# Performance work log

Measured on AMD Instinct MI355X. Metric: run time of the kernel, lower is better.

## Reference

```python
import jax, jax.numpy as jnp
import numpy as np
import math

B, T, D = 2, 2048, 1024
NH = 16
HD = D // NH


def setup_inputs() -> dict:
    key = jax.random.key(0)
    k1, k2, k3 = jax.random.split(key, 3)
    scale = 0.02
    x = jax.random.normal(k1, (B, T, D), dtype=jnp.float32)
    Wqkv = jax.random.normal(k2, (D, 3 * D), dtype=jnp.float32) * scale
    bqkv = jnp.zeros((3 * D,), dtype=jnp.float32)
    Wproj = jax.random.normal(k3, (D, D), dtype=jnp.float32) * scale
    bproj = jnp.zeros((D,), dtype=jnp.float32)
    return {"x": x, "Wqkv": Wqkv, "bqkv": bqkv, "Wproj": Wproj, "bproj": bproj}


def reference(x, Wqkv, bqkv, Wproj, bproj):
    b, t, c = x.shape
    qkv = x @ Wqkv + bqkv                      # [B,T,3D]
    q, k, v = jnp.split(qkv, 3, axis=2)
    # [B,T,NH,HD] -> [B,NH,T,HD]
    q = q.reshape(b, t, NH, HD).transpose(0, 2, 1, 3)
    k = k.reshape(b, t, NH, HD).transpose(0, 2, 1, 3)
    v = v.reshape(b, t, NH, HD).transpose(0, 2, 1, 3)
    att = jnp.einsum('bhqd,bhkd->bhqk', q, k) / math.sqrt(HD)  # [B,NH,T,T]
    causal = jnp.tril(jnp.ones((t, t), dtype=bool))
    att = jnp.where(causal, att, -jnp.inf)
    att = jax.nn.softmax(att, axis=-1)
    y = jnp.einsum('bhqk,bhkd->bhqd', att, v)  # [B,NH,T,HD]
    y = y.transpose(0, 2, 1, 3).reshape(b, t, c)
    return y @ Wproj + bproj
```

## Files before the change

kernel.cpp:

```cpp
#include <hip/hip_runtime.h>
#include <hip/hip_bf16.h>

#define B_   2
#define T_   2048
#define D_   1024
#define NH_  16
#define HD_  64
#define MROWS (B_*T_)
#define HEADELEMS (B_*NH_*T_*HD_)

#define QSCALE 0.180336880f

typedef unsigned short u16;
typedef unsigned int   u32;

typedef float f32x4  __attribute__((ext_vector_type(4)));
typedef short bf16x8 __attribute__((ext_vector_type(8)));

#define GLP(g, l) __builtin_amdgcn_global_load_lds(                         \
    (const __attribute__((address_space(1))) void*)(g),                     \
    (__attribute__((address_space(3))) void*)(l), 16, 0, 0)

struct Fc { static constexpr bool value = false; };
struct Tc { static constexpr bool value = true;  };

__device__ __forceinline__ u16 f2bf(float f) {
    u32 x = __float_as_uint(f);
    u32 r = (x + 0x7fffu + ((x >> 16) & 1u)) >> 16;
    return (u16)r;
}
__device__ __forceinline__ u32 pkbf2(float a, float b) {
    __hip_bfloat162 h = __float22bfloat162_rn(make_float2(a, b));
    union { __hip_bfloat162 h2; u32 u; } cv; cv.h2 = h; return cv.u;
}

__device__ __forceinline__ void transpose_tile(const float* in, u16* out,
                                               int K, int N, int bx, int by,
                                               int t, float (*Ts)[65])
{
    const int n0 = bx * 64;
    const int k0 = by * 64;
    #pragma unroll
    for (int pass = 0; pass < 4; pass++) {
        const int r = pass * 16 + (t >> 4);
        const int c = (t & 15) * 4;
        float4 v = *(const float4*)(in + (size_t)(k0 + r) * N + n0 + c);
        Ts[r][c] = v.x; Ts[r][c+1] = v.y; Ts[r][c+2] = v.z; Ts[r][c+3] = v.w;
    }
    __syncthreads();
    #pragma unroll
    for (int pass = 0; pass < 2; pass++) {
        const int nn = pass * 32 + (t >> 3);
        const int kk = (t & 7) * 8;
        u16 o[8];
        #pragma unroll
        for (int j = 0; j < 8; j++) o[j] = f2bf(Ts[kk + j][nn]);
        *(uint4*)(out + (size_t)(n0 + nn) * K + k0 + kk) = *(const uint4*)o;
    }
}

__global__ __launch_bounds__(256)
void prep_kernel(const float* __restrict__ x, const float* __restrict__ Wqkv,
                 const float* __restrict__ Wproj, u16* __restrict__ xb,
                 u16* __restrict__ WqkvT, u16* __restrict__ WprojT)
{
    __shared__ float Ts[64][65];
    const int bid = blockIdx.x;
    const int t   = threadIdx.x;
    if (bid < 4096) {
        int i = bid * 256 + t;
        float4 v = ((const float4*)x)[i];
        ushort4 o;
        o.x = f2bf(v.x); o.y = f2bf(v.y); o.z = f2bf(v.z); o.w = f2bf(v.w);
        ((ushort4*)xb)[i] = o;
    } else if (bid < 4096 + 768) {
        int tb = bid - 4096;
        transpose_tile(Wqkv, WqkvT, D_, 3*D_, tb % 48, tb / 48, t, Ts);
    } else {
        int tb = bid - 4864;
        transpose_tile(Wproj, WprojT, D_, D_, tb % 16, tb / 16, t, Ts);
    }
}

__global__ __launch_bounds__(256)
void transpose_conv_kernel(const float* __restrict__ in, u16* __restrict__ out,
                           int K, int N)
{
    __shared__ float Ts[64][65];
    transpose_tile(in, out, K, N, blockIdx.x, blockIdx.y, threadIdx.x, Ts);
}

template <int MODE>
__global__ __launch_bounds__(256)
void gemm_mfma(const u16* __restrict__ A, const u16* __restrict__ BT,
               const float* __restrict__ bias, void* __restrict__ outv,
               int M, int N, int K)
{
    __shared__ u16 As[128][64];
    __shared__ u16 Bs[128][64];

    const int t    = threadIdx.x;
    const int wave = t >> 6;
    const int lane = t & 63;
    const int l16  = lane & 15;
    const int quad = lane >> 4;

    const int m0 = blockIdx.y * 128;
    const int n0 = blockIdx.x * 128;
    const int mb = (wave >> 1) * 64;
    const int nb = (wave & 1) * 64;

    const int srow = lane >> 3;
    const int sseg = ((lane & 7) ^ srow) * 8;

    const int rw = wave * 32;
    const u16* gA = A  + (size_t)(m0 + rw + srow) * K + sseg;
    const u16* gB = BT + (size_t)(n0 + rw + srow) * K + sseg;

    const int fragcol = (quad ^ (l16 & 7)) * 8;

    f32x4 acc[4][4];
    #pragma unroll
    for (int i = 0; i < 4; i++)
        #pragma unroll
        for (int j = 0; j < 4; j++) acc[i][j] = (f32x4){0,0,0,0};

    for (int k0 = 0; k0 < K; k0 += 64) {
        __syncthreads();
        GLP(gA + k0,            &As[rw     ][0]);
        GLP(gA + k0 +  8*K,     &As[rw +  8][0]);
        GLP(gA + k0 + 16*K,     &As[rw + 16][0]);
        GLP(gA + k0 + 24*K,     &As[rw + 24][0]);
        GLP(gB + k0,            &Bs[rw     ][0]);
        GLP(gB + k0 +  8*K,     &Bs[rw +  8][0]);
        GLP(gB + k0 + 16*K,     &Bs[rw + 16][0]);
        GLP(gB + k0 + 24*K,     &Bs[rw + 24][0]);
        __syncthreads();

        #pragma unroll
        for (int kk = 0; kk < 2; kk++) {
            const int fc = fragcol ^ (kk << 5);
            bf16x8 af[4], bfr[4];
            #pragma unroll
            for (int i = 0; i < 4; i++)
                af[i] = *(const bf16x8*)&As[mb + i*16 + l16][fc];
            #pragma unroll
            for (int j = 0; j < 4; j++)
                bfr[j] = *(const bf16x8*)&Bs[nb + j*16 + l16][fc];

            #pragma unroll
            for (int i = 0; i < 4; i++)
                #pragma unroll
                for (int j = 0; j < 4; j++)
                    acc[i][j] = __builtin_amdgcn_mfma_f32_16x16x32_bf16(
                        af[i], bfr[j], acc[i][j], 0, 0, 0);
        }
    }

    if (MODE == 0) {
        #pragma unroll
        for (int j = 0; j < 4; j++) {
            const int n = n0 + nb + j*16 + l16;
            const float bv = bias[n];
            #pragma unroll
            for (int i = 0; i < 4; i++) {
                #pragma unroll
                for (int r = 0; r < 4; r++) {
                    const int m = m0 + mb + i*16 + quad*4 + r;
                    ((float*)outv)[(size_t)m * N + n] = acc[i][j][r] + bv;
                }
            }
        }
    } else {
        const int sec = n0 >> 10;
        const int b   = m0 >> 11;
        const int tb  = m0 & 2047;
        if (sec < 2) {
            const float qs = (sec == 0) ? QSCALE : 1.f;
            #pragma unroll
            for (int j = 0; j < 4; j++) {
                const int n  = n0 + nb + j*16 + l16;
                const float bv = bias[n];
                const int dd = n & 1023;
                const int h  = dd >> 6;
                const int hd = dd & 63;
                u16* op = (u16*)outv + (size_t)sec * HEADELEMS
                        + ((size_t)(b*NH_ + h)) * T_ * HD_ + hd;
                #pragma unroll
                for (int i = 0; i < 4; i++) {
                    #pragma unroll
                    for (int r = 0; r < 4; r++) {
                        const int tt = tb + mb + i*16 + quad*4 + r;
                        op[(size_t)tt * HD_] = f2bf((acc[i][j][r] + bv) * qs);
                    }
                }
            }
        } else {
            #pragma unroll
            for (int j = 0; j < 4; j++) {
                const int n  = n0 + nb + j*16 + l16;
                const float bv = bias[n];
                const int dd = n & 1023;
                const int h  = dd >> 6;
                const int hd = dd & 63;
                u16* vp = (u16*)outv + (size_t)2 * HEADELEMS
                        + ((size_t)(b*NH_ + h)) * T_ * HD_
                        + (size_t)hd * T_ + tb + mb;
                #pragma unroll
                for (int i = 0; i < 4; i++) {
                    u16 o[4];
                    #pragma unroll
                    for (int r = 0; r < 4; r++) o[r] = f2bf(acc[i][j][r] + bv);
                    *(uint2*)(vp + i*16 + quad*4) = *(const uint2*)o;
                }
            }
        }
    }
}

__global__ __launch_bounds__(256)
void attn_mfma_kernel(const u16* __restrict__ Q, const u16* __restrict__ K,
                      const u16* __restrict__ VT, u16* __restrict__ y1)
{
    __shared__ u16 Ks[2][64][64];
    __shared__ u16 Vs[2][64][64];

    const int t    = threadIdx.x;
    const int wave = t >> 6;
    const int lane = t & 63;
    const int l16  = lane & 15;
    const int quad = lane >> 4;

    const int hb = blockIdx.x;
    const int yy = blockIdx.y;
    const int a  = yy & 7, g = yy >> 3;
    const int qt = (g == 0) ? 31 - a : (g == 1) ? 16 + a
                 : (g == 2) ? 15 - a : a;
    const int b  = hb >> 4;
    const int h  = hb & 15;
    const size_t base = (size_t)hb * T_ * HD_;

    const int qw0 = qt * 64 + wave * 16;

    bf16x8 qf[2];
    {
        const u16* qp = Q + base + (size_t)(qw0 + l16) * HD_ + quad * 8;
        qf[0] = *(const bf16x8*)(qp);
        qf[1] = *(const bf16x8*)(qp + 32);
    }

    bf16x8 onesf;
    #pragma unroll
    for (int i = 0; i < 8; i++) onesf[i] = (short)0x3F80;

    f32x4 o[4];
    #pragma unroll
    for (int d = 0; d < 4; d++) o[d] = (f32x4){0,0,0,0};
    f32x4 accl = (f32x4){0,0,0,0};

    const int nsteps = qt + 1;

    const int srow = t >> 3;
    const int scol = (t & 7) * 8;
    const int sst  = (((t & 7) ^ (srow & 7)) * 8);

    const int fs0 = (quad ^ (l16 & 7)) * 8;
    const int fs1 = fs0 ^ 32;

    const int srcA  = l16 + ((quad & 1) << 5);
    const int srcB  = srcA + 16;
    const bool selhi = (quad >> 1) != 0;

    uint4 kr0, kr1, vr0, vr1;
    {
        const u16* kp = K + base + (size_t)srow * HD_ + scol;
        kr0 = *(const uint4*)kp;
        kr1 = *(const uint4*)(kp + 32 * HD_);
        const u16* vp = VT + base + (size_t)srow * T_ + scol;
        vr0 = *(const uint4*)vp;
        vr1 = *(const uint4*)(vp + 32 * T_);
        *(uint4*)&Ks[0][srow][sst]      = kr0;
        *(uint4*)&Ks[0][srow + 32][sst] = kr1;
        *(uint4*)&Vs[0][srow][sst]      = vr0;
        *(uint4*)&Vs[0][srow + 32][sst] = vr1;
    }
    __syncthreads();

    auto compute_tile = [&](int cur, int k0, auto mc) {
        constexpr bool MASKED = decltype(mc)::value;
        f32x4 st[4];
        __builtin_amdgcn_s_setprio(1);
        #pragma unroll
        for (int j = 0; j < 4; j++) {
            bf16x8 kf0 = *(const bf16x8*)&Ks[cur][j*16 + l16][fs0];
            bf16x8 kf1 = *(const bf16x8*)&Ks[cur][j*16 + l16][fs1];
            f32x4 z = {0,0,0,0};
            z = __builtin_amdgcn_mfma_f32_16x16x32_bf16(kf0, qf[0], z, 0, 0, 0);
            st[j] = __builtin_amdgcn_mfma_f32_16x16x32_bf16(kf1, qf[1], z, 0, 0, 0);
        }
        __builtin_amdgcn_s_setprio(0);

        u32 p01[4], p23[4];
        const int qi = qw0 + l16;
        #pragma unroll
        for (int j = 0; j < 4; j++) {
            const int kb = k0 + j*16 + quad*4;
            float e0 = __builtin_amdgcn_exp2f(st[j][0]);
            float e1 = __builtin_amdgcn_exp2f(st[j][1]);
            float e2 = __builtin_amdgcn_exp2f(st[j][2]);
            float e3 = __builtin_amdgcn_exp2f(st[j][3]);
            if (MASKED) {
                if (kb + 0 > qi) e0 = 0.f;
                if (kb + 1 > qi) e1 = 0.f;
                if (kb + 2 > qi) e2 = 0.f;
                if (kb + 3 > qi) e3 = 0.f;
            }
            p01[j] = pkbf2(e0, e1);
            p23[j] = pkbf2(e2, e3);
        }

        bf16x8 pf[2];
        #pragma unroll
        for (int c = 0; c < 2; c++) {
            u32 t0, t1, r01, r23, r45, r67;
            t0 = (u32)__shfl((int)p01[2*c],   srcA);
            t1 = (u32)__shfl((int)p01[2*c+1], srcA);
            r01 = selhi ? t1 : t0;
            t0 = (u32)__shfl((int)p23[2*c],   srcA);
            t1 = (u32)__shfl((int)p23[2*c+1], srcA);
            r23 = selhi ? t1 : t0;
            t0 = (u32)__shfl((int)p01[2*c],   srcB);
            t1 = (u32)__shfl((int)p01[2*c+1], srcB);
            r45 = selhi ? t1 : t0;
            t0 = (u32)__shfl((int)p23[2*c],   srcB);
            t1 = (u32)__shfl((int)p23[2*c+1], srcB);
            r67 = selhi ? t1 : t0;
            union { u32 u[4]; bf16x8 v; } pk;
            pk.u[0] = r01; pk.u[1] = r23; pk.u[2] = r45; pk.u[3] = r67;
            pf[c] = pk.v;
        }
        __builtin_amdgcn_s_setprio(1);
        accl = __builtin_amdgcn_mfma_f32_16x16x32_bf16(pf[0], onesf, accl, 0, 0, 0);
        accl = __builtin_amdgcn_mfma_f32_16x16x32_bf16(pf[1], onesf, accl, 0, 0, 0);
        #pragma unroll
        for (int d = 0; d < 4; d++) {
            bf16x8 v0 = *(const bf16x8*)&Vs[cur][d*16 + l16][fs0];
            bf16x8 v1 = *(const bf16x8*)&Vs[cur][d*16 + l16][fs1];
            o[d] = __builtin_amdgcn_mfma_f32_16x16x32_bf16(pf[0], v0, o[d], 0, 0, 0);
            o[d] = __builtin_amdgcn_mfma_f32_16x16x32_bf16(pf[1], v1, o[d], 0, 0, 0);
        }
        __builtin_amdgcn_s_setprio(0);
    };

    for (int kt = 0; kt < nsteps; kt++) {
        const int cur = kt & 1;
        const int k0  = kt * 64;
        const bool have_next = (kt + 1 < nsteps);

        if (have_next) {
            const u16* kp = K + base + (size_t)(k0 + 64 + srow) * HD_ + scol;
            kr0 = *(const uint4*)kp;
            kr1 = *(const uint4*)(kp + 32 * HD_);
            const u16* vp = VT + base + (size_t)srow * T_ + k0 + 64 + scol;
            vr0 = *(const uint4*)vp;
            vr1 = *(const uint4*)(vp + 32 * T_);
        }

        if (kt < qt) compute_tile(cur, k0, Fc{});
        else         compute_tile(cur, k0, Tc{});

        if (have_next) {
            const int nxt = cur ^ 1;
            *(uint4*)&Ks[nxt][srow][sst]      = kr0;
            *(uint4*)&Ks[nxt][srow + 32][sst] = kr1;
            *(uint4*)&Vs[nxt][srow][sst]      = vr0;
            *(uint4*)&Vs[nxt][srow + 32][sst] = vr1;
            __syncthreads();
        }
    }

    #pragma unroll
    for (int r = 0; r < 4; r++) {
        const float inv = 1.f / accl[r];
        const int qi = qw0 + quad*4 + r;
        u16* yp = y1 + ((size_t)(b * T_ + qi)) * D_ + h * HD_ + l16;
        yp[0]  = f2bf(o[0][r] * inv);
        yp[16] = f2bf(o[1][r] * inv);
        yp[32] = f2bf(o[2][r] * inv);
        yp[48] = f2bf(o[3][r] * inv);
    }
}

extern "C" void kernel_launch(void* const* d_in, const int* in_sizes, int n_in,
                              void* d_out, int out_size, void* d_ws, size_t ws_size,
                              hipStream_t stream)
{
    const float* x     = (const float*)d_in[0];
    const float* Wqkv  = (const float*)d_in[1];
    const float* bqkv  = (const float*)d_in[2];
    const float* Wproj = (const float*)d_in[3];
    const float* bproj = (const float*)d_in[4];

    u16* scratch = (u16*)d_out;
    u16* xb      = scratch;
    u16* WqkvT   = scratch + (size_t)MROWS * D_;

    const size_t Y1E = (size_t)MROWS * D_;
    const size_t WPE = (size_t)D_ * D_;

    u16* qkv = (u16*)d_ws;
    u16* Qp  = qkv;
    u16* Kp  = qkv + (size_t)HEADELEMS;
    u16* Vtp = qkv + (size_t)2 * HEADELEMS;

    const bool huge = ws_size >= ((size_t)3 * HEADELEMS + Y1E + WPE) * 2;
    const bool big  = ws_size >= ((size_t)3 * HEADELEMS + Y1E) * 2;

    u16* y1b    = big ? qkv + (size_t)3 * HEADELEMS : scratch;
    u16* y1g    = big ? y1b : Vtp;
    u16* WprojT = huge ? qkv + (size_t)3 * HEADELEMS + Y1E : Kp;

    prep_kernel<<<huge ? 5120 : 4864, 256, 0, stream>>>(
        x, Wqkv, Wproj, xb, WqkvT, WprojT);

    gemm_mfma<1><<<dim3(3*D_/128, MROWS/128), 256, 0, stream>>>(
        xb, WqkvT, bqkv, (void*)qkv, MROWS, 3*D_, D_);

    attn_mfma_kernel<<<dim3(NH_*B_, T_/64), 256, 0, stream>>>(Qp, Kp, Vtp, y1b);

    if (!huge)
        transpose_conv_kernel<<<dim3(D_/64, D_/64), 256, 0, stream>>>(
            Wproj, WprojT, D_, D_);

    if (!big)
        (void)hipMemcpyAsync(y1g, y1b, Y1E * sizeof(u16),
                             hipMemcpyDeviceToDevice, stream);

    gemm_mfma<0><<<dim3(D_/128, MROWS/128), 256, 0, stream>>>(
        y1g, WprojT, bproj, d_out, MROWS, D_, D_);
}
```

Measured before the change: 195.2 us.

## Double-buffer GEMM LDS tiles and remap blocks for XCD-aware scheduling

The MFMA GEMM now keeps two LDS buffers and prefetches the next K tile with global_load_lds while computing on the current one, using manual vmcnt waits and barriers instead of two syncthreads per step. The grid is flattened to 1D and block IDs are permuted so consecutive blocks on the same XCD work on adjacent tiles, aiming for better L2 reuse. The staging layout also changes so each wave loads interleaved rows. This doubles LDS use per block, which may lower occupancy, and the hardcoded `idp & 31` M-tile mapping assumes exactly 32 M tiles.

```diff
diff --git a/kernel.cpp b/kernel.cpp
--- a/kernel.cpp
+++ b/kernel.cpp
@@ -96,8 +96,8 @@
                const float* __restrict__ bias, void* __restrict__ outv,
                int M, int N, int K)
 {
-    __shared__ u16 As[128][64];
-    __shared__ u16 Bs[128][64];
+    __shared__ u16 As[2][128][64];
+    __shared__ u16 Bs[2][128][64];
 
     const int t    = threadIdx.x;
     const int wave = t >> 6;
@@ -105,17 +105,23 @@
     const int l16  = lane & 15;
     const int quad = lane >> 4;
 
-    const int m0 = blockIdx.y * 128;
-    const int n0 = blockIdx.x * 128;
+    const int flat = blockIdx.x;
+    const int cpx  = gridDim.x >> 3;
+    const int idp  = (flat & 7) * cpx + (flat >> 3);
+    const int bx   = idp >> 5;
+    const int by   = idp & 31;
+
+    const int m0 = by * 128;
+    const int n0 = bx * 128;
     const int mb = (wave >> 1) * 64;
     const int nb = (wave & 1) * 64;
 
-    const int srow = lane >> 3;
-    const int sseg = ((lane & 7) ^ srow) * 8;
-
-    const int rw = wave * 32;
-    const u16* gA = A  + (size_t)(m0 + rw + srow) * K + sseg;
-    const u16* gB = BT + (size_t)(n0 + rw + srow) * K + sseg;
+    const int srow = t >> 3;
+    const int sseg = ((t & 7) ^ (srow & 7)) * 8;
+    const int rw8  = wave * 8;
+
+    const u16* gA = A  + (size_t)(m0 + srow) * K + sseg;
+    const u16* gB = BT + (size_t)(n0 + srow) * K + sseg;
 
     const int fragcol = (quad ^ (l16 & 7)) * 8;
 
@@ -125,17 +131,34 @@
         #pragma unroll
         for (int j = 0; j < 4; j++) acc[i][j] = (f32x4){0,0,0,0};
 
-    for (int k0 = 0; k0 < K; k0 += 64) {
-        __syncthreads();
-        GLP(gA + k0,            &As[rw     ][0]);
-        GLP(gA + k0 +  8*K,     &As[rw +  8][0]);
-        GLP(gA + k0 + 16*K,     &As[rw + 16][0]);
-        GLP(gA + k0 + 24*K,     &As[rw + 24][0]);
-        GLP(gB + k0,            &Bs[rw     ][0]);
-        GLP(gB + k0 +  8*K,     &Bs[rw +  8][0]);
-        GLP(gB + k0 + 16*K,     &Bs[rw + 16][0]);
-        GLP(gB + k0 + 24*K,     &Bs[rw + 24][0]);
-        __syncthreads();
+    auto STAGE = [&](int buf, int k0) {
+        GLP(gA + k0,          &As[buf][rw8     ][0]);
+        GLP(gA + k0 + 32*K,   &As[buf][rw8 + 32][0]);
+        GLP(gA + k0 + 64*K,   &As[buf][rw8 + 64][0]);
+        GLP(gA + k0 + 96*K,   &As[buf][rw8 + 96][0]);
+        GLP(gB + k0,          &Bs[buf][rw8     ][0]);
+        GLP(gB + k0 + 32*K,   &Bs[buf][rw8 + 32][0]);
+        GLP(gB + k0 + 64*K,   &Bs[buf][rw8 + 64][0]);
+        GLP(gB + k0 + 96*K,   &Bs[buf][rw8 + 96][0]);
+    };
+
+    const int nk = K >> 6;
+
+    STAGE(0, 0);
+    asm volatile("s_waitcnt vmcnt(0)" ::: "memory");
+    __builtin_amdgcn_s_barrier();
+
+    for (int kt = 0; kt < nk; ++kt) {
+        const int cur = kt & 1;
+        const bool have_next = (kt + 1 < nk);
+
+        if (have_next) {
+            STAGE(cur ^ 1, (kt + 1) << 6);
+            asm volatile("s_waitcnt vmcnt(8)" ::: "memory");
+        } else {
+            asm volatile("s_waitcnt vmcnt(0)" ::: "memory");
+        }
+        __builtin_amdgcn_s_barrier();
 
         #pragma unroll
         for (int kk = 0; kk < 2; kk++) {
@@ -143,10 +166,10 @@
             bf16x8 af[4], bfr[4];
             #pragma unroll
             for (int i = 0; i < 4; i++)
-                af[i] = *(const bf16x8*)&As[mb + i*16 + l16][fc];
+                af[i] = *(const bf16x8*)&As[cur][mb + i*16 + l16][fc];
             #pragma unroll
             for (int j = 0; j < 4; j++)
-                bfr[j] = *(const bf16x8*)&Bs[nb + j*16 + l16][fc];
+                bfr[j] = *(const bf16x8*)&Bs[cur][nb + j*16 + l16][fc];
 
             #pragma unroll
             for (int i = 0; i < 4; i++)
@@ -154,6 +177,11 @@
                 for (int j = 0; j < 4; j++)
                     acc[i][j] = __builtin_amdgcn_mfma_f32_16x16x32_bf16(
                         af[i], bfr[j], acc[i][j], 0, 0, 0);
+        }
+
+        if (have_next) {
+            asm volatile("s_waitcnt lgkmcnt(0)" ::: "memory");
+            __builtin_amdgcn_s_barrier();
         }
     }
 
@@ -423,7 +451,7 @@
     prep_kernel<<<huge ? 5120 : 4864, 256, 0, stream>>>(
         x, Wqkv, Wproj, xb, WqkvT, WprojT);
 
-    gemm_mfma<1><<<dim3(3*D_/128, MROWS/128), 256, 0, stream>>>(
+    gemm_mfma<1><<<768, 256, 0, stream>>>(
         xb, WqkvT, bqkv, (void*)qkv, MROWS, 3*D_, D_);
 
     attn_mfma_kernel<<<dim3(NH_*B_, T_/64), 256, 0, stream>>>(Qp, Kp, Vtp, y1b);
@@ -436,6 +464,6 @@
         (void)hipMemcpyAsync(y1g, y1b, Y1E * sizeof(u16),
                              hipMemcpyDeviceToDevice, stream);
 
-    gemm_mfma<0><<<dim3(D_/128, MROWS/128), 256, 0, stream>>>(
+    gemm_mfma<0><<<256, 256, 0, stream>>>(
         y1g, WprojT, bproj, d_out, MROWS, D_, D_);
 }
```

After: 194.5 us. About the same (-0.4%).
